# Performance work log

Measured on AMD Instinct MI355X. Metric: run time of the kernel, lower is better.

Reference implementation:

```python
import jax, jax.numpy as jnp
import numpy as np

N = 100000   # nodes
E = 1600000  # edges
IN = 64      # in_channels
H = 64       # hidden_channels
OUT = 2      # out_channels
EPS = 1e-5   # BatchNorm eps


def setup_inputs() -> dict:
    key = jax.random.key(0)
    ks = jax.random.split(key, 14)
    x = jax.random.normal(ks[0], (N, IN), dtype=jnp.float32)
    edge_index = jax.random.randint(ks[1], (2, E), 0, N, dtype=jnp.int64)

    def lin(k, shape, fan_in):
        return (jax.random.normal(k, shape, dtype=jnp.float32) / np.float32(np.sqrt(fan_in)))

    return {
        "x": x,
        "edge_index": edge_index,
        "W0": lin(ks[2], (IN, H), IN),
        "b0": jnp.zeros((H,), jnp.float32),
        "g0": jnp.ones((H,), jnp.float32),
        "be0": jnp.zeros((H,), jnp.float32),
        "W1": lin(ks[3], (H, H), H),
        "b1": jnp.zeros((H,), jnp.float32),
        "g1": jnp.ones((H,), jnp.float32),
        "be1": jnp.zeros((H,), jnp.float32),
        "W2": lin(ks[4], (H, OUT), H),
        "b2": jnp.zeros((OUT,), jnp.float32),
    }


def _gcn_conv(h_in, W, b, src, dst, norm):
    # GCNConv: linear transform, then D^-1/2 (A + I) D^-1/2 aggregation, then bias
    h = h_in @ W                                   # [N, d_out]
    msg = h[src] * norm[:, None]                   # gather + scale, [E+N, d_out]
    agg = jax.ops.segment_sum(msg, dst, num_segments=N)
    return agg + b


def _batch_norm(h, gamma, beta):
    # training-mode BatchNorm1d over the node dimension (biased variance)
    mean = jnp.mean(h, axis=0)
    var = jnp.mean(jnp.square(h - mean), axis=0)
    return (h - mean) * jax.lax.rsqrt(var + EPS) * gamma + beta


def reference(x, edge_index, W0, b0, g0, be0, W1, b1, g1, be1, W2, b2):
    loop = jnp.arange(N, dtype=edge_index.dtype)
    src = jnp.concatenate([edge_index[0], loop])   # self loops appended
    dst = jnp.concatenate([edge_index[1], loop])
    deg = jax.ops.segment_sum(jnp.ones_like(dst, dtype=jnp.float32), dst, num_segments=N)
    dinv = jax.lax.rsqrt(deg)                      # deg >= 1 due to self loops
    norm = dinv[src] * dinv[dst]                   # [E+N]

    h = jax.nn.relu(_batch_norm(_gcn_conv(x, W0, b0, src, dst, norm), g0, be0))
    h_res = h
    h = jax.nn.relu(_batch_norm(_gcn_conv(h, W1, b1, src, dst, norm), g1, be1))
    h = h + h_res                                  # residual add
    out = _gcn_conv(h, W2, b2, src, dst, norm)     # [N, OUT]
    return out
```

## Files before the change

kernel.cpp:

```cpp
#include <hip/hip_runtime.h>


#define NN 100000
#define NE 1600000
#define NBUCK 1563
#define NBLK 256
#define CHUNK 6250
#define MAXB 2048

typedef unsigned short ushort_t;
typedef __attribute__((ext_vector_type(8))) short bf16x8;
typedef __attribute__((ext_vector_type(4))) float f32x4;

__device__ __forceinline__ ushort_t f2bf(float f) {
    unsigned u = __float_as_uint(f);
    unsigned r = u + 0x7FFFu + ((u >> 16) & 1u);
    return (ushort_t)(r >> 16);
}
__device__ __forceinline__ float bflo(unsigned u) { return __uint_as_float(u << 16); }
__device__ __forceinline__ float bfhi(unsigned u) { return __uint_as_float(u & 0xFFFF0000u); }

__launch_bounds__(1024)
__global__ void kA_hist(const int* __restrict__ dst, int* __restrict__ H) {
    __shared__ int h[NBUCK];
    int t = threadIdx.x, blk = blockIdx.x;
    for (int b = t; b < NBUCK; b += 1024) h[b] = 0;
    __syncthreads();
    int e0 = blk * CHUNK;
    for (int e = e0 + t; e < e0 + CHUNK; e += 1024) atomicAdd(&h[dst[e] >> 6], 1);
    __syncthreads();
    for (int b = t; b < NBUCK; b += 1024) H[b * NBLK + blk] = h[b];
}
__launch_bounds__(256)
__global__ void kB1(const int* __restrict__ H, int* __restrict__ bsum) {
    __shared__ int sh[256];
    int b = blockIdx.x, t = threadIdx.x;
    sh[t] = H[b * NBLK + t];
    __syncthreads();
    for (int s = 128; s; s >>= 1) {
        if (t < s) sh[t] += sh[t + s];
        __syncthreads();
    }
    if (t == 0) bsum[b] = sh[0];
}
__global__ void kB2(const int* __restrict__ bsum, int* __restrict__ bbase) {
    __shared__ int part[256];
    int t = threadIdx.x;
    int loc[7];
    int s = 0;
#pragma unroll
    for (int k = 0; k < 7; ++k) {
        int i = t * 7 + k;
        int v = (i < NBUCK) ? bsum[i] : 0;
        loc[k] = s;
        s += v;
    }
    part[t] = s;
    __syncthreads();
    if (t == 0) {
        int acc = 0;
        for (int i = 0; i < 256; ++i) { int v = part[i]; part[i] = acc; acc += v; }
        bbase[NBUCK] = acc;
    }
    __syncthreads();
    int base = part[t];
#pragma unroll
    for (int k = 0; k < 7; ++k) {
        int i = t * 7 + k;
        if (i < NBUCK) bbase[i] = base + loc[k];
    }
}
__launch_bounds__(256)
__global__ void kB3(int* __restrict__ H, const int* __restrict__ bbase) {
    __shared__ int sh[256];
    int b = blockIdx.x, t = threadIdx.x;
    sh[t] = H[b * NBLK + t];
    __syncthreads();
    if (t == 0) {
        int acc = bbase[b];
        for (int i = 0; i < 256; ++i) { int v = sh[i]; sh[i] = acc; acc += v; }
    }
    __syncthreads();
    H[b * NBLK + t] = sh[t];
}
__launch_bounds__(256)
__global__ void kC_scatter(const int* __restrict__ src, const int* __restrict__ dst,
                           const int* __restrict__ O, unsigned int* __restrict__ sp) {
    __shared__ int cur[NBUCK];
    int t = threadIdx.x, blk = blockIdx.x;
    for (int b = t; b < NBUCK; b += 256) cur[b] = O[b * NBLK + blk];
    __syncthreads();
    int e0 = blk * CHUNK;
    for (int e = e0 + t; e < e0 + CHUNK; e += 256) {
        int d = dst[e], s = src[e];
        int p = atomicAdd(&cur[d >> 6], 1);
        sp[p] = ((unsigned int)(d & 63) << 24) | (unsigned int)s;
    }
}
__launch_bounds__(256)
__global__ void kD2_fin(const unsigned int* __restrict__ sp, const int* __restrict__ bbase,
                        int* __restrict__ csrc, int* __restrict__ rowstart,
                        int* __restrict__ cntg, float* __restrict__ dinv) {
    __shared__ int cnt[64], ofs[64], cur[64];
    __shared__ int tmp[MAXB];
    int b = blockIdx.x, t = threadIdx.x;
    int beg = bbase[b], end = bbase[b + 1], n = end - beg;
    if (t < 64) cnt[t] = 0;
    __syncthreads();
    for (int i = beg + t; i < end; i += 256) atomicAdd(&cnt[sp[i] >> 24], 1);
    __syncthreads();
    if (t == 0) {
        int acc = 0;
        for (int k = 0; k < 64; ++k) { int v = cnt[k]; ofs[k] = acc; cur[k] = acc; acc += v; }
    }
    __syncthreads();
    int node = b * 64 + t;
    if (t < 64 && node < NN) {
        rowstart[node] = beg + ofs[t];
        cntg[node] = cnt[t];
        dinv[node] = rsqrtf((float)(cnt[t] + 1));
    }
    if (n <= MAXB) {
        for (int i = beg + t; i < end; i += 256) {
            unsigned int v = sp[i];
            int p = atomicAdd(&cur[v >> 24], 1);
            tmp[p] = (int)(v & 0xFFFFFFu);
        }
        __syncthreads();
        for (int i = t; i < n; i += 256) csrc[beg + i] = tmp[i];
    } else {
        for (int i = beg + t; i < end; i += 256) {
            unsigned int v = sp[i];
            int p = atomicAdd(&cur[v >> 24], 1);
            csrc[beg + p] = (int)(v & 0xFFFFFFu);
        }
    }
}

template <int MODE>
__launch_bounds__(256, 4)
__global__ void k_gemm_mfma(const float* __restrict__ X, const float* __restrict__ W,
                            const float* __restrict__ stats, const float* __restrict__ g,
                            const float* __restrict__ be, const float* __restrict__ dinv,
                            ushort_t* __restrict__ Yb, float* __restrict__ side) {
    int t = threadIdx.x;
    int lane = t & 63, wv = t >> 6;
    int m = lane & 15;
    int kg = lane >> 4;

    bf16x8 bfr[4][2];
#pragma unroll
    for (int ct = 0; ct < 4; ++ct)
#pragma unroll
        for (int kf = 0; kf < 2; ++kf)
#pragma unroll
            for (int e = 0; e < 8; ++e) {
                int k = kf * 32 + kg * 8 + e;
                bfr[ct][kf][e] = (short)f2bf(W[k * 64 + ct * 16 + m]);
            }

    float sc[2][8], sh[2][8];
    if (MODE == 1) {
#pragma unroll
        for (int kf = 0; kf < 2; ++kf) {
            int k0 = kf * 32 + kg * 8;
            const f32x4* s4 = (const f32x4*)(stats + k0);
            const f32x4* q4 = (const f32x4*)(stats + 64 + k0);
            const f32x4* g4 = (const f32x4*)(g + k0);
            const f32x4* b4 = (const f32x4*)(be + k0);
#pragma unroll
            for (int h = 0; h < 2; ++h) {
                f32x4 sv = s4[h], qv = q4[h], gv = g4[h], bv = b4[h];
#pragma unroll
                for (int e2 = 0; e2 < 4; ++e2) {
                    float mean = sv[e2] * (1.0f / NN);
                    float var = qv[e2] * (1.0f / NN) - mean * mean;
                    float s = gv[e2] * rsqrtf(var + 1e-5f);
                    sc[kf][h * 4 + e2] = s;
                    sh[kf][h * 4 + e2] = bv[e2] - mean * s;
                }
            }
        }
    }

    int tile0 = blockIdx.x * 8 + wv * 2;
#pragma unroll
    for (int tt = 0; tt < 2; ++tt) {
        int row0 = (tile0 + tt) * 16;
        if (row0 >= NN) break;
        long arow = row0 + m;
        bf16x8 afr[2];
#pragma unroll
        for (int kf = 0; kf < 2; ++kf) {
            const f32x4* xp = (const f32x4*)(X + arow * 64 + kf * 32 + kg * 8);
            f32x4 v0 = xp[0], v1 = xp[1];
            if (MODE == 1) {
#pragma unroll
                for (int e = 0; e < 4; ++e) {
                    v0[e] = fmaxf(fmaf(v0[e], sc[kf][e], sh[kf][e]), 0.f);
                    v1[e] = fmaxf(fmaf(v1[e], sc[kf][e + 4], sh[kf][e + 4]), 0.f);
                }
                f32x4* sp2 = (f32x4*)(side + arow * 64 + kf * 32 + kg * 8);
                sp2[0] = v0;
                sp2[1] = v1;
            }
#pragma unroll
            for (int e = 0; e < 4; ++e) {
                afr[kf][e] = (short)f2bf(v0[e]);
                afr[kf][e + 4] = (short)f2bf(v1[e]);
            }
        }
        f32x4 acc0 = {0.f, 0.f, 0.f, 0.f}, acc1 = acc0, acc2 = acc0, acc3 = acc0;
        acc0 = __builtin_amdgcn_mfma_f32_16x16x32_bf16(afr[0], bfr[0][0], acc0, 0, 0, 0);
        acc0 = __builtin_amdgcn_mfma_f32_16x16x32_bf16(afr[1], bfr[0][1], acc0, 0, 0, 0);
        acc1 = __builtin_amdgcn_mfma_f32_16x16x32_bf16(afr[0], bfr[1][0], acc1, 0, 0, 0);
        acc1 = __builtin_amdgcn_mfma_f32_16x16x32_bf16(afr[1], bfr[1][1], acc1, 0, 0, 0);
        acc2 = __builtin_amdgcn_mfma_f32_16x16x32_bf16(afr[0], bfr[2][0], acc2, 0, 0, 0);
        acc2 = __builtin_amdgcn_mfma_f32_16x16x32_bf16(afr[1], bfr[2][1], acc2, 0, 0, 0);
        acc3 = __builtin_amdgcn_mfma_f32_16x16x32_bf16(afr[0], bfr[3][0], acc3, 0, 0, 0);
        acc3 = __builtin_amdgcn_mfma_f32_16x16x32_bf16(afr[1], bfr[3][1], acc3, 0, 0, 0);
#pragma unroll
        for (int r = 0; r < 4; ++r) {
            int grow = row0 + kg * 4 + r;
            float dd = dinv[grow];
            long gb = (long)grow * 64 + m;
            Yb[gb] = f2bf(dd * acc0[r]);
            Yb[gb + 16] = f2bf(dd * acc1[r]);
            Yb[gb + 32] = f2bf(dd * acc2[r]);
            Yb[gb + 48] = f2bf(dd * acc3[r]);
        }
    }
}

#define ACC8(q)                                                   \
    acc0.x += bflo(q.x); acc0.y += bfhi(q.x);                     \
    acc0.z += bflo(q.y); acc0.w += bfhi(q.y);                     \
    acc1.x += bflo(q.z); acc1.y += bfhi(q.z);                     \
    acc1.z += bflo(q.w); acc1.w += bfhi(q.w);

__launch_bounds__(256)
__global__ void k_agg_csr(const ushort_t* __restrict__ Yb, const int* __restrict__ rowstart,
                          const int* __restrict__ cnt, const int* __restrict__ csrc,
                          const float* __restrict__ dinv, float* __restrict__ agg) {
    int wid = (blockIdx.x * blockDim.x + threadIdx.x) >> 6;
    int lane = threadIdx.x & 63;
    if (wid >= NN) return;
    int grp = lane >> 3;
    int l8 = lane & 7;
    int beg = rowstart[wid], n = cnt[wid];
    float4 acc0 = {0.f, 0.f, 0.f, 0.f}, acc1 = {0.f, 0.f, 0.f, 0.f};
    if (grp == 0) {
        uint4 q = ((const uint4*)(Yb + (long)wid * 64))[l8];
        ACC8(q);
    }
    int j = grp;
    for (; j + 8 < n; j += 16) {
        int s0 = csrc[beg + j];
        int s1 = csrc[beg + j + 8];
        uint4 q0 = ((const uint4*)(Yb + (long)s0 * 64))[l8];
        uint4 q1 = ((const uint4*)(Yb + (long)s1 * 64))[l8];
        ACC8(q0);
        ACC8(q1);
    }
    if (j < n) {
        int s = csrc[beg + j];
        uint4 q = ((const uint4*)(Yb + (long)s * 64))[l8];
        ACC8(q);
    }
#pragma unroll
    for (int m = 8; m <= 32; m <<= 1) {
        acc0.x += __shfl_xor(acc0.x, m);
        acc0.y += __shfl_xor(acc0.y, m);
        acc0.z += __shfl_xor(acc0.z, m);
        acc0.w += __shfl_xor(acc0.w, m);
        acc1.x += __shfl_xor(acc1.x, m);
        acc1.y += __shfl_xor(acc1.y, m);
        acc1.z += __shfl_xor(acc1.z, m);
        acc1.w += __shfl_xor(acc1.w, m);
    }
    if (grp == 0) {
        float d = dinv[wid];
        float4 r0 = {acc0.x * d, acc0.y * d, acc0.z * d, acc0.w * d};
        float4 r1 = {acc1.x * d, acc1.y * d, acc1.z * d, acc1.w * d};
        ((float4*)(agg + (long)wid * 64))[l8 * 2] = r0;
        ((float4*)(agg + (long)wid * 64))[l8 * 2 + 1] = r1;
    }
}

__launch_bounds__(256)
__global__ void k_bn_stats(const float* __restrict__ X, float* __restrict__ stats) {
    __shared__ float sh[512];
    int t = threadIdx.x;
    int c = t & 63, rr = t >> 6;
    float sum = 0.f, sq = 0.f;
    for (int r = blockIdx.x * 4 + rr; r < NN; r += gridDim.x * 4) {
        float v = X[r * 64 + c];
        sum += v;
        sq = fmaf(v, v, sq);
    }
    sh[t] = sum;
    sh[256 + t] = sq;
    __syncthreads();
    if (t < 64) {
        float s = sh[t] + sh[t + 64] + sh[t + 128] + sh[t + 192];
        float q = sh[256 + t] + sh[320 + t] + sh[384 + t] + sh[448 + t];
        atomicAdd(&stats[t], s);
        atomicAdd(&stats[64 + t], q);
    }
}

__launch_bounds__(256)
__global__ void k_gemm_out2(const float* __restrict__ X, const float* __restrict__ stats,
                            const float* __restrict__ g, const float* __restrict__ be,
                            const float* __restrict__ R, const float* __restrict__ W2,
                            const float* __restrict__ dinv, float* __restrict__ Tp) {
    int t = threadIdx.x;
    int lane = t & 63, wv = t >> 6;
    int row = blockIdx.x * 4 + wv;
    if (row >= NN) return;
    float mean = stats[lane] * (1.0f / NN);
    float var = stats[64 + lane] * (1.0f / NN) - mean * mean;
    float scale = g[lane] * rsqrtf(var + 1e-5f);
    float shift = be[lane] - mean * scale;
    float w0 = W2[lane * 2], w1 = W2[lane * 2 + 1];
    float v = X[row * 64 + lane];
    v = fmaxf(fmaf(v, scale, shift), 0.f) + R[row * 64 + lane];
    float p0 = v * w0, p1 = v * w1;
#pragma unroll
    for (int s = 32; s; s >>= 1) {
        p0 += __shfl_xor(p0, s);
        p1 += __shfl_xor(p1, s);
    }
    if (lane == 0) {
        float d = dinv[row];
        Tp[row * 2] = d * p0;
        Tp[row * 2 + 1] = d * p1;
    }
}

__launch_bounds__(256)
__global__ void k_out_csr(const float* __restrict__ Tp, const int* __restrict__ rowstart,
                          const int* __restrict__ cnt, const int* __restrict__ csrc,
                          const float* __restrict__ dinv, const float* __restrict__ b2,
                          float* __restrict__ out) {
    int id = blockIdx.x * blockDim.x + threadIdx.x;
    int node = id >> 3, l = id & 7;
    if (node >= NN) return;
    int beg = rowstart[node], n = cnt[node];
    float a0 = 0.f, a1 = 0.f;
    if (l == 0) { a0 = Tp[node * 2]; a1 = Tp[node * 2 + 1]; }
    for (int j = l; j < n; j += 8) {
        int s = csrc[beg + j];
        a0 += Tp[s * 2];
        a1 += Tp[s * 2 + 1];
    }
#pragma unroll
    for (int m = 1; m < 8; m <<= 1) {
        a0 += __shfl_xor(a0, m);
        a1 += __shfl_xor(a1, m);
    }
    if (l == 0) {
        float d = dinv[node];
        out[node * 2] = d * a0 + b2[0];
        out[node * 2 + 1] = d * a1 + b2[1];
    }
}

extern "C" void kernel_launch(void* const* d_in, const int* in_sizes, int n_in,
                              void* d_out, int out_size, void* d_ws, size_t ws_size,
                              hipStream_t stream) {
    const float* x   = (const float*)d_in[0];
    const int*   ei  = (const int*)d_in[1];
    const int*   src = ei;
    const int*   dst = ei + NE;
    const float* W0  = (const float*)d_in[2];
    const float* g0  = (const float*)d_in[4];
    const float* be0 = (const float*)d_in[5];
    const float* W1  = (const float*)d_in[6];
    const float* g1  = (const float*)d_in[8];
    const float* be1 = (const float*)d_in[9];
    const float* W2  = (const float*)d_in[10];
    const float* b2  = (const float*)d_in[11];
    float* out = (float*)d_out;

    int*   H      = (int*)d_ws;
    int*   bsum   = H + NBUCK * NBLK;
    int*   bbase  = bsum + 2048;
    unsigned int* sp = (unsigned int*)(bbase + 2048);
    int*   csrc   = (int*)(sp + NE);
    int*   rowstart = csrc + NE;
    int*   cntg   = rowstart + NN;
    float* dinv   = (float*)(cntg + NN);
    ushort_t* Ab  = (ushort_t*)(dinv + NN);
    float* B      = (float*)(Ab + NN * 64);
    float* C      = B + NN * 64;
    float* Tp     = C + NN * 64;
    float* stats0 = Tp + NN * 2;
    float* stats1 = stats0 + 128;

    hipMemsetAsync(stats0, 0, 256 * sizeof(float), stream);

    kA_hist<<<NBLK, 1024, 0, stream>>>(dst, H);
    kB1<<<NBUCK, 256, 0, stream>>>(H, bsum);
    kB2<<<1, 256, 0, stream>>>(bsum, bbase);
    kB3<<<NBUCK, 256, 0, stream>>>(H, bbase);
    kC_scatter<<<NBLK, 256, 0, stream>>>(src, dst, H, sp);
    kD2_fin<<<NBUCK, 256, 0, stream>>>(sp, bbase, csrc, rowstart, cntg, dinv);

    int mfmaGrid = 782;
    int aggGrid  = (NN * 64) / 256;

    k_gemm_mfma<0><<<mfmaGrid, 256, 0, stream>>>(x, W0, nullptr, nullptr, nullptr, dinv, Ab, nullptr);
    k_agg_csr<<<aggGrid, 256, 0, stream>>>(Ab, rowstart, cntg, csrc, dinv, B);
    k_bn_stats<<<1024, 256, 0, stream>>>(B, stats0);

    k_gemm_mfma<1><<<mfmaGrid, 256, 0, stream>>>(B, W1, stats0, g0, be0, dinv, Ab, C);
    k_agg_csr<<<aggGrid, 256, 0, stream>>>(Ab, rowstart, cntg, csrc, dinv, B);
    k_bn_stats<<<1024, 256, 0, stream>>>(B, stats1);

    k_gemm_out2<<<(NN + 3) / 4, 256, 0, stream>>>(B, stats1, g1, be1, C, W2, dinv, Tp);
    k_out_csr<<<(NN * 8 + 255) / 256, 256, 0, stream>>>(Tp, rowstart, cntg, csrc, dinv, b2, out);
}
```

Measured before the change: 344.6 us.

## Sub-bin CSR buckets by source range to improve gather locality

The counting-sort histogram, scan and scatter now bin edges by destination bucket times seven source-range chunks, so within each destination bucket the edges come out grouped by source index range. The aim is to make the later neighbour-row gathers in the aggregation kernels hit nearby memory and improve cache reuse. In exchange the histogram and scan handle seven times more bins, and the bucket workspace now reuses the B and C buffers to save memory. The bounds check in the aggregation kernel is also dropped, since the grid exactly covers all nodes.

```diff
diff --git a/kernel.cpp b/kernel.cpp
--- a/kernel.cpp
+++ b/kernel.cpp
@@ -4,6 +4,8 @@
 #define NN 100000
 #define NE 1600000
 #define NBUCK 1563
+#define NCH 7
+#define NBIN (NBUCK * NCH)
 #define NBLK 256
 #define CHUNK 6250
 #define MAXB 2048
@@ -21,15 +23,19 @@
 __device__ __forceinline__ float bfhi(unsigned u) { return __uint_as_float(u & 0xFFFF0000u); }
 
 __launch_bounds__(1024)
-__global__ void kA_hist(const int* __restrict__ dst, int* __restrict__ H) {
-    __shared__ int h[NBUCK];
+__global__ void kA_hist(const int* __restrict__ src, const int* __restrict__ dst,
+                        int* __restrict__ H) {
+    __shared__ int h[NBIN];
     int t = threadIdx.x, blk = blockIdx.x;
-    for (int b = t; b < NBUCK; b += 1024) h[b] = 0;
+    for (int b = t; b < NBIN; b += 1024) h[b] = 0;
     __syncthreads();
     int e0 = blk * CHUNK;
-    for (int e = e0 + t; e < e0 + CHUNK; e += 1024) atomicAdd(&h[dst[e] >> 6], 1);
-    __syncthreads();
-    for (int b = t; b < NBUCK; b += 1024) H[b * NBLK + blk] = h[b];
+    for (int e = e0 + t; e < e0 + CHUNK; e += 1024) {
+        int bin = (dst[e] >> 6) * NCH + (src[e] >> 14);
+        atomicAdd(&h[bin], 1);
+    }
+    __syncthreads();
+    for (int b = t; b < NBIN; b += 1024) H[b * NBLK + blk] = h[b];
 }
 __launch_bounds__(256)
 __global__ void kB1(const int* __restrict__ H, int* __restrict__ bsum) {
@@ -43,32 +49,23 @@
     }
     if (t == 0) bsum[b] = sh[0];
 }
+#define SCAN_PER 43
 __global__ void kB2(const int* __restrict__ bsum, int* __restrict__ bbase) {
     __shared__ int part[256];
     int t = threadIdx.x;
-    int loc[7];
+    int lo = t * SCAN_PER, hi = min(lo + SCAN_PER, NBIN);
     int s = 0;
-#pragma unroll
-    for (int k = 0; k < 7; ++k) {
-        int i = t * 7 + k;
-        int v = (i < NBUCK) ? bsum[i] : 0;
-        loc[k] = s;
-        s += v;
-    }
+    for (int i = lo; i < hi; ++i) s += bsum[i];
     part[t] = s;
     __syncthreads();
     if (t == 0) {
         int acc = 0;
         for (int i = 0; i < 256; ++i) { int v = part[i]; part[i] = acc; acc += v; }
-        bbase[NBUCK] = acc;
-    }
-    __syncthreads();
-    int base = part[t];
-#pragma unroll
-    for (int k = 0; k < 7; ++k) {
-        int i = t * 7 + k;
-        if (i < NBUCK) bbase[i] = base + loc[k];
-    }
+        bbase[NBIN] = acc;
+    }
+    __syncthreads();
+    int acc = part[t];
+    for (int i = lo; i < hi; ++i) { bbase[i] = acc; acc += bsum[i]; }
 }
 __launch_bounds__(256)
 __global__ void kB3(int* __restrict__ H, const int* __restrict__ bbase) {
@@ -86,14 +83,15 @@
 __launch_bounds__(256)
 __global__ void kC_scatter(const int* __restrict__ src, const int* __restrict__ dst,
                            const int* __restrict__ O, unsigned int* __restrict__ sp) {
-    __shared__ int cur[NBUCK];
+    __shared__ int cur[NBIN];
     int t = threadIdx.x, blk = blockIdx.x;
-    for (int b = t; b < NBUCK; b += 256) cur[b] = O[b * NBLK + blk];
+    for (int b = t; b < NBIN; b += 256) cur[b] = O[b * NBLK + blk];
     __syncthreads();
     int e0 = blk * CHUNK;
     for (int e = e0 + t; e < e0 + CHUNK; e += 256) {
         int d = dst[e], s = src[e];
-        int p = atomicAdd(&cur[d >> 6], 1);
+        int bin = (d >> 6) * NCH + (s >> 14);
+        int p = atomicAdd(&cur[bin], 1);
         sp[p] = ((unsigned int)(d & 63) << 24) | (unsigned int)s;
     }
 }
@@ -104,7 +102,7 @@
     __shared__ int cnt[64], ofs[64], cur[64];
     __shared__ int tmp[MAXB];
     int b = blockIdx.x, t = threadIdx.x;
-    int beg = bbase[b], end = bbase[b + 1], n = end - beg;
+    int beg = bbase[b * NCH], end = bbase[b * NCH + NCH], n = end - beg;
     if (t < 64) cnt[t] = 0;
     __syncthreads();
     for (int i = beg + t; i < end; i += 256) atomicAdd(&cnt[sp[i] >> 24], 1);
@@ -244,7 +242,6 @@
                           const float* __restrict__ dinv, float* __restrict__ agg) {
     int wid = (blockIdx.x * blockDim.x + threadIdx.x) >> 6;
     int lane = threadIdx.x & 63;
-    if (wid >= NN) return;
     int grp = lane >> 3;
     int l8 = lane & 7;
     int beg = rowstart[wid], n = cnt[wid];
@@ -383,10 +380,7 @@
     const float* b2  = (const float*)d_in[11];
     float* out = (float*)d_out;
 
-    int*   H      = (int*)d_ws;
-    int*   bsum   = H + NBUCK * NBLK;
-    int*   bbase  = bsum + 2048;
-    unsigned int* sp = (unsigned int*)(bbase + 2048);
+    unsigned int* sp = (unsigned int*)d_ws;
     int*   csrc   = (int*)(sp + NE);
     int*   rowstart = csrc + NE;
     int*   cntg   = rowstart + NN;
@@ -398,12 +392,16 @@
     float* stats0 = Tp + NN * 2;
     float* stats1 = stats0 + 128;
 
+    int* H     = (int*)B;
+    int* bsum  = (int*)C;
+    int* bbase = (int*)C + 16384;
+
     hipMemsetAsync(stats0, 0, 256 * sizeof(float), stream);
 
-    kA_hist<<<NBLK, 1024, 0, stream>>>(dst, H);
-    kB1<<<NBUCK, 256, 0, stream>>>(H, bsum);
+    kA_hist<<<NBLK, 1024, 0, stream>>>(src, dst, H);
+    kB1<<<NBIN, 256, 0, stream>>>(H, bsum);
     kB2<<<1, 256, 0, stream>>>(bsum, bbase);
-    kB3<<<NBUCK, 256, 0, stream>>>(H, bbase);
+    kB3<<<NBIN, 256, 0, stream>>>(H, bbase);
     kC_scatter<<<NBLK, 256, 0, stream>>>(src, dst, H, sp);
     kD2_fin<<<NBUCK, 256, 0, stream>>>(sp, bbase, csrc, rowstart, cntg, dinv);
 
```

Measured after the change: 423.9 us. 1.23x slower.

## Store aggregated activations in bf16 and recompute residual instead of writing side buffer

Applied to the files above, without the earlier changes.

The aggregation output is now packed to bf16 instead of fp32, which halves the bytes written by the aggregation and read by the BN-stats, GEMM and output kernels. The layer-1 GEMM no longer writes the fp32 normalized residual (side buffer). The final kernel instead recomputes BN0+ReLU from the bf16 layer-0 aggregate and adds it to BN1+ReLU of the layer-1 aggregate. This cuts memory traffic at the cost of an extra bf16 rounding on BN inputs and statistics, which may affect accuracy.

```diff
diff --git a/kernel.cpp b/kernel.cpp
--- a/kernel.cpp
+++ b/kernel.cpp
@@ -19,6 +19,9 @@
 }
 __device__ __forceinline__ float bflo(unsigned u) { return __uint_as_float(u << 16); }
 __device__ __forceinline__ float bfhi(unsigned u) { return __uint_as_float(u & 0xFFFF0000u); }
+__device__ __forceinline__ unsigned pk(float a, float b) {
+    return (unsigned)f2bf(a) | ((unsigned)f2bf(b) << 16);
+}
 
 __launch_bounds__(1024)
 __global__ void kA_hist(const int* __restrict__ dst, int* __restrict__ H) {
@@ -139,10 +142,10 @@
 
 template <int MODE>
 __launch_bounds__(256, 4)
-__global__ void k_gemm_mfma(const float* __restrict__ X, const float* __restrict__ W,
+__global__ void k_gemm_mfma(const void* __restrict__ Xv, const float* __restrict__ W,
                             const float* __restrict__ stats, const float* __restrict__ g,
                             const float* __restrict__ be, const float* __restrict__ dinv,
-                            ushort_t* __restrict__ Yb, float* __restrict__ side) {
+                            ushort_t* __restrict__ Yb) {
     int t = threadIdx.x;
     int lane = t & 63, wv = t >> 6;
     int m = lane & 15;
@@ -163,22 +166,14 @@
     if (MODE == 1) {
 #pragma unroll
         for (int kf = 0; kf < 2; ++kf) {
-            int k0 = kf * 32 + kg * 8;
-            const f32x4* s4 = (const f32x4*)(stats + k0);
-            const f32x4* q4 = (const f32x4*)(stats + 64 + k0);
-            const f32x4* g4 = (const f32x4*)(g + k0);
-            const f32x4* b4 = (const f32x4*)(be + k0);
-#pragma unroll
-            for (int h = 0; h < 2; ++h) {
-                f32x4 sv = s4[h], qv = q4[h], gv = g4[h], bv = b4[h];
-#pragma unroll
-                for (int e2 = 0; e2 < 4; ++e2) {
-                    float mean = sv[e2] * (1.0f / NN);
-                    float var = qv[e2] * (1.0f / NN) - mean * mean;
-                    float s = gv[e2] * rsqrtf(var + 1e-5f);
-                    sc[kf][h * 4 + e2] = s;
-                    sh[kf][h * 4 + e2] = bv[e2] - mean * s;
-                }
+#pragma unroll
+            for (int e = 0; e < 8; ++e) {
+                int k = kf * 32 + kg * 8 + e;
+                float mean = stats[k] * (1.0f / NN);
+                float var = stats[64 + k] * (1.0f / NN) - mean * mean;
+                float s = g[k] * rsqrtf(var + 1e-5f);
+                sc[kf][e] = s;
+                sh[kf][e] = be[k] - mean * s;
             }
         }
     }
@@ -192,22 +187,22 @@
         bf16x8 afr[2];
 #pragma unroll
         for (int kf = 0; kf < 2; ++kf) {
-            const f32x4* xp = (const f32x4*)(X + arow * 64 + kf * 32 + kg * 8);
-            f32x4 v0 = xp[0], v1 = xp[1];
-            if (MODE == 1) {
+            if (MODE == 0) {
+                const f32x4* xp = (const f32x4*)((const float*)Xv + arow * 64 + kf * 32 + kg * 8);
+                f32x4 v0 = xp[0], v1 = xp[1];
 #pragma unroll
                 for (int e = 0; e < 4; ++e) {
-                    v0[e] = fmaxf(fmaf(v0[e], sc[kf][e], sh[kf][e]), 0.f);
-                    v1[e] = fmaxf(fmaf(v1[e], sc[kf][e + 4], sh[kf][e + 4]), 0.f);
+                    afr[kf][e] = (short)f2bf(v0[e]);
+                    afr[kf][e + 4] = (short)f2bf(v1[e]);
                 }
-                f32x4* sp2 = (f32x4*)(side + arow * 64 + kf * 32 + kg * 8);
-                sp2[0] = v0;
-                sp2[1] = v1;
-            }
-#pragma unroll
-            for (int e = 0; e < 4; ++e) {
-                afr[kf][e] = (short)f2bf(v0[e]);
-                afr[kf][e + 4] = (short)f2bf(v1[e]);
+            } else {
+                const uint4* xp = (const uint4*)((const ushort_t*)Xv + arow * 64 + kf * 32 + kg * 8);
+                uint4 q = *xp;
+                float f[8] = {bflo(q.x), bfhi(q.x), bflo(q.y), bfhi(q.y),
+                              bflo(q.z), bfhi(q.z), bflo(q.w), bfhi(q.w)};
+#pragma unroll
+                for (int e = 0; e < 8; ++e)
+                    afr[kf][e] = (short)f2bf(fmaxf(fmaf(f[e], sc[kf][e], sh[kf][e]), 0.f));
             }
         }
         f32x4 acc0 = {0.f, 0.f, 0.f, 0.f}, acc1 = acc0, acc2 = acc0, acc3 = acc0;
@@ -241,10 +236,9 @@
 __launch_bounds__(256)
 __global__ void k_agg_csr(const ushort_t* __restrict__ Yb, const int* __restrict__ rowstart,
                           const int* __restrict__ cnt, const int* __restrict__ csrc,
-                          const float* __restrict__ dinv, float* __restrict__ agg) {
+                          const float* __restrict__ dinv, ushort_t* __restrict__ aggb) {
     int wid = (blockIdx.x * blockDim.x + threadIdx.x) >> 6;
     int lane = threadIdx.x & 63;
-    if (wid >= NN) return;
     int grp = lane >> 3;
     int l8 = lane & 7;
     int beg = rowstart[wid], n = cnt[wid];
@@ -280,58 +274,79 @@
     }
     if (grp == 0) {
         float d = dinv[wid];
-        float4 r0 = {acc0.x * d, acc0.y * d, acc0.z * d, acc0.w * d};
-        float4 r1 = {acc1.x * d, acc1.y * d, acc1.z * d, acc1.w * d};
-        ((float4*)(agg + (long)wid * 64))[l8 * 2] = r0;
-        ((float4*)(agg + (long)wid * 64))[l8 * 2 + 1] = r1;
-    }
-}
-
-__launch_bounds__(256)
-__global__ void k_bn_stats(const float* __restrict__ X, float* __restrict__ stats) {
-    __shared__ float sh[512];
+        uint4 o;
+        o.x = pk(acc0.x * d, acc0.y * d);
+        o.y = pk(acc0.z * d, acc0.w * d);
+        o.z = pk(acc1.x * d, acc1.y * d);
+        o.w = pk(acc1.z * d, acc1.w * d);
+        ((uint4*)(aggb + (long)wid * 64))[l8] = o;
+    }
+}
+
+__launch_bounds__(256)
+__global__ void k_bn_stats(const ushort_t* __restrict__ Xb, float* __restrict__ stats) {
+    __shared__ float sh[1024];
     int t = threadIdx.x;
-    int c = t & 63, rr = t >> 6;
-    float sum = 0.f, sq = 0.f;
-    for (int r = blockIdx.x * 4 + rr; r < NN; r += gridDim.x * 4) {
-        float v = X[r * 64 + c];
-        sum += v;
-        sq = fmaf(v, v, sq);
-    }
-    sh[t] = sum;
-    sh[256 + t] = sq;
-    __syncthreads();
-    if (t < 64) {
-        float s = sh[t] + sh[t + 64] + sh[t + 128] + sh[t + 192];
-        float q = sh[256 + t] + sh[320 + t] + sh[384 + t] + sh[448 + t];
-        atomicAdd(&stats[t], s);
-        atomicAdd(&stats[64 + t], q);
-    }
-}
-
-__launch_bounds__(256)
-__global__ void k_gemm_out2(const float* __restrict__ X, const float* __restrict__ stats,
-                            const float* __restrict__ g, const float* __restrict__ be,
-                            const float* __restrict__ R, const float* __restrict__ W2,
-                            const float* __restrict__ dinv, float* __restrict__ Tp) {
+    int c2 = t & 31, rr = t >> 5;
+    float s0 = 0.f, s1 = 0.f, q0 = 0.f, q1 = 0.f;
+    for (int r = blockIdx.x * 8 + rr; r < NN; r += gridDim.x * 8) {
+        unsigned q = ((const unsigned*)(Xb + (long)r * 64))[c2];
+        float v0 = bflo(q), v1 = bfhi(q);
+        s0 += v0; s1 += v1;
+        q0 = fmaf(v0, v0, q0); q1 = fmaf(v1, v1, q1);
+    }
+    sh[t] = s0; sh[256 + t] = s1; sh[512 + t] = q0; sh[768 + t] = q1;
+    __syncthreads();
+    if (t < 32) {
+        float S0 = 0.f, S1 = 0.f, Q0 = 0.f, Q1 = 0.f;
+#pragma unroll
+        for (int r = 0; r < 8; ++r) {
+            S0 += sh[r * 32 + t];
+            S1 += sh[256 + r * 32 + t];
+            Q0 += sh[512 + r * 32 + t];
+            Q1 += sh[768 + r * 32 + t];
+        }
+        atomicAdd(&stats[2 * t], S0);
+        atomicAdd(&stats[2 * t + 1], S1);
+        atomicAdd(&stats[64 + 2 * t], Q0);
+        atomicAdd(&stats[64 + 2 * t + 1], Q1);
+    }
+}
+
+__launch_bounds__(256)
+__global__ void k_gemm_out2(const ushort_t* __restrict__ Cb, const ushort_t* __restrict__ Bb,
+                            const float* __restrict__ stats0, const float* __restrict__ g0,
+                            const float* __restrict__ be0, const float* __restrict__ stats1,
+                            const float* __restrict__ g1, const float* __restrict__ be1,
+                            const float* __restrict__ W2, const float* __restrict__ dinv,
+                            float* __restrict__ Tp) {
     int t = threadIdx.x;
-    int lane = t & 63, wv = t >> 6;
-    int row = blockIdx.x * 4 + wv;
-    if (row >= NN) return;
-    float mean = stats[lane] * (1.0f / NN);
-    float var = stats[64 + lane] * (1.0f / NN) - mean * mean;
-    float scale = g[lane] * rsqrtf(var + 1e-5f);
-    float shift = be[lane] - mean * scale;
-    float w0 = W2[lane * 2], w1 = W2[lane * 2 + 1];
-    float v = X[row * 64 + lane];
-    v = fmaxf(fmaf(v, scale, shift), 0.f) + R[row * 64 + lane];
-    float p0 = v * w0, p1 = v * w1;
-#pragma unroll
-    for (int s = 32; s; s >>= 1) {
+    int c2 = t & 31;
+    int row = blockIdx.x * 8 + (t >> 5);
+    int ch0 = 2 * c2, ch1 = ch0 + 1;
+    float m00 = stats0[ch0] * (1.0f / NN), m01 = stats0[ch1] * (1.0f / NN);
+    float sc00 = g0[ch0] * rsqrtf(stats0[64 + ch0] * (1.0f / NN) - m00 * m00 + 1e-5f);
+    float sc01 = g0[ch1] * rsqrtf(stats0[64 + ch1] * (1.0f / NN) - m01 * m01 + 1e-5f);
+    float sh00 = be0[ch0] - m00 * sc00, sh01 = be0[ch1] - m01 * sc01;
+    float m10 = stats1[ch0] * (1.0f / NN), m11 = stats1[ch1] * (1.0f / NN);
+    float sc10 = g1[ch0] * rsqrtf(stats1[64 + ch0] * (1.0f / NN) - m10 * m10 + 1e-5f);
+    float sc11 = g1[ch1] * rsqrtf(stats1[64 + ch1] * (1.0f / NN) - m11 * m11 + 1e-5f);
+    float sh10 = be1[ch0] - m10 * sc10, sh11 = be1[ch1] - m11 * sc11;
+    float w00 = W2[ch0 * 2], w01 = W2[ch0 * 2 + 1];
+    float w10 = W2[ch1 * 2], w11 = W2[ch1 * 2 + 1];
+
+    unsigned qc = ((const unsigned*)(Cb + (long)row * 64))[c2];
+    unsigned qb = ((const unsigned*)(Bb + (long)row * 64))[c2];
+    float v0 = fmaxf(fmaf(bflo(qc), sc10, sh10), 0.f) + fmaxf(fmaf(bflo(qb), sc00, sh00), 0.f);
+    float v1 = fmaxf(fmaf(bfhi(qc), sc11, sh11), 0.f) + fmaxf(fmaf(bfhi(qb), sc01, sh01), 0.f);
+    float p0 = v0 * w00 + v1 * w10;
+    float p1 = v0 * w01 + v1 * w11;
+#pragma unroll
+    for (int s = 16; s; s >>= 1) {
         p0 += __shfl_xor(p0, s);
         p1 += __shfl_xor(p1, s);
     }
-    if (lane == 0) {
+    if (c2 == 0) {
         float d = dinv[row];
         Tp[row * 2] = d * p0;
         Tp[row * 2 + 1] = d * p1;
@@ -392,9 +407,9 @@
     int*   cntg   = rowstart + NN;
     float* dinv   = (float*)(cntg + NN);
     ushort_t* Ab  = (ushort_t*)(dinv + NN);
-    float* B      = (float*)(Ab + NN * 64);
-    float* C      = B + NN * 64;
-    float* Tp     = C + NN * 64;
+    ushort_t* Bb  = Ab + NN * 64;
+    ushort_t* Cb  = Bb + NN * 64;
+    float* Tp     = (float*)(Cb + NN * 64);
     float* stats0 = Tp + NN * 2;
     float* stats1 = stats0 + 128;
 
@@ -410,14 +425,14 @@
     int mfmaGrid = 782;
     int aggGrid  = (NN * 64) / 256;
 
-    k_gemm_mfma<0><<<mfmaGrid, 256, 0, stream>>>(x, W0, nullptr, nullptr, nullptr, dinv, Ab, nullptr);
-    k_agg_csr<<<aggGrid, 256, 0, stream>>>(Ab, rowstart, cntg, csrc, dinv, B);
-    k_bn_stats<<<1024, 256, 0, stream>>>(B, stats0);
-
-    k_gemm_mfma<1><<<mfmaGrid, 256, 0, stream>>>(B, W1, stats0, g0, be0, dinv, Ab, C);
-    k_agg_csr<<<aggGrid, 256, 0, stream>>>(Ab, rowstart, cntg, csrc, dinv, B);
-    k_bn_stats<<<1024, 256, 0, stream>>>(B, stats1);
-
-    k_gemm_out2<<<(NN + 3) / 4, 256, 0, stream>>>(B, stats1, g1, be1, C, W2, dinv, Tp);
+    k_gemm_mfma<0><<<mfmaGrid, 256, 0, stream>>>(x, W0, nullptr, nullptr, nullptr, dinv, Ab);
+    k_agg_csr<<<aggGrid, 256, 0, stream>>>(Ab, rowstart, cntg, csrc, dinv, Bb);
+    k_bn_stats<<<1024, 256, 0, stream>>>(Bb, stats0);
+
+    k_gemm_mfma<1><<<mfmaGrid, 256, 0, stream>>>(Bb, W1, stats0, g0, be0, dinv, Ab);
+    k_agg_csr<<<aggGrid, 256, 0, stream>>>(Ab, rowstart, cntg, csrc, dinv, Cb);
+    k_bn_stats<<<1024, 256, 0, stream>>>(Cb, stats1);
+
+    k_gemm_out2<<<NN / 8, 256, 0, stream>>>(Cb, Bb, stats0, g0, be0, stats1, g1, be1, W2, dinv, Tp);
     k_out_csr<<<(NN * 8 + 255) / 256, 256, 0, stream>>>(Tp, rowstart, cntg, csrc, dinv, b2, out);
 }
```

Result: slower. 384.0 us (+11.4%).
